# Kernel tuning notes

Measured on AMD Instinct MI355X. Metric: run time of the kernel, lower is better.

The kernel has to match this reference:

```python
import jax, jax.numpy as jnp
import numpy as np

F = 128  # num_features
N = 200000

def setup_inputs() -> dict:
    key = jax.random.key(0)
    ks = jax.random.split(key, 9)
    s = 0.05
    inp = {
        "node_feat": jax.random.normal(ks[0], (N, 4 * F), dtype=jnp.float32),
        "U_w": jax.random.normal(ks[1], (F, F), dtype=jnp.float32) * s,
        "U_b": jax.random.normal(ks[2], (F,), dtype=jnp.float32) * s,
        "V_w": jax.random.normal(ks[3], (F, F), dtype=jnp.float32) * s,
        "V_b": jax.random.normal(ks[4], (F,), dtype=jnp.float32) * s,
        "m1_w": jax.random.normal(ks[5], (2 * F, F), dtype=jnp.float32) * s,
        "m1_b": jax.random.normal(ks[6], (F,), dtype=jnp.float32) * s,
        "m2_w": jax.random.normal(ks[7], (F, 3 * F), dtype=jnp.float32) * s,
        "m2_b": jax.random.normal(ks[8], (3 * F,), dtype=jnp.float32) * s,
    }
    return inp

def reference(node_feat, U_w, U_b, V_w, V_b, m1_w, m1_b, m2_w, m2_b):
    node_scalar = node_feat[:, :F]                       # [N, F]
    node_vector = node_feat[:, F:].reshape(-1, 3, F)     # [N, 3, F]
    Uv = jnp.einsum('ncf,fg->ncg', node_vector, U_w) + U_b  # [N, 3, F]
    Vv = jnp.einsum('ncf,fg->ncg', node_vector, V_w) + V_b  # [N, 3, F]
    Vv_norm = jnp.linalg.norm(Vv, axis=1)                # [N, F]
    mlp_in = jnp.concatenate((Vv_norm, node_scalar), axis=1)  # [N, 2F]
    h = jax.nn.silu(mlp_in @ m1_w + m1_b)                # [N, F]
    mlp_out = h @ m2_w + m2_b                            # [N, 3F]
    a_vv, a_sv, a_ss = jnp.split(mlp_out, 3, axis=1)
    delta_v = a_vv[:, None, :] * Uv                      # [N, 3, F]
    inner_prod = jnp.sum(Uv * Vv, axis=1)                # [N, F]
    delta_s = a_sv * inner_prod + a_ss                   # [N, F]
    residual = jnp.concatenate([delta_s, delta_v.reshape(-1, 3 * F)], axis=1)
    return node_feat + residual
```

## Files before the change

### kernel.cpp

```cpp
#include <hip/hip_runtime.h>


#define NT 16
#define STRA 136
#define STRS 136
#define STRN 136
#define STRH 136

typedef __attribute__((ext_vector_type(8))) short bf16x8;
typedef __attribute__((ext_vector_type(4))) short short4v;
typedef __attribute__((ext_vector_type(4))) float f32x4;

#define MFMA16(a, b, c) __builtin_amdgcn_mfma_f32_16x16x32_bf16(a, b, c, 0, 0, 0)

__device__ __forceinline__ short f2bf(float x) {
    union { float f; unsigned u; } v; v.f = x;
    unsigned r = v.u + 0x7fffu + ((v.u >> 16) & 1u);
    return (short)(r >> 16);
}

__global__ void prep_weights(const float* __restrict__ Uw, const float* __restrict__ Vw,
                             const float* __restrict__ m1w, const float* __restrict__ m2w,
                             short* __restrict__ ws) {
    int idx = blockIdx.x * 256 + threadIdx.x;
    if (idx < 16384) {
        int g = idx >> 7, k = idx & 127;
        ws[idx]         = f2bf(Uw[k * 128 + g]);
        ws[16384 + idx] = f2bf(Vw[k * 128 + g]);
    } else if (idx < 49152) {
        int j = idx - 16384;
        int g = j >> 8, k = j & 255;
        ws[32768 + j] = f2bf(m1w[k * 128 + g]);
    } else if (idx < 98304) {
        int j = idx - 49152;
        int g = j >> 7, k = j & 127;
        ws[65536 + j] = f2bf(m2w[k * 384 + g]);
    }
}

__global__ __launch_bounds__(256, 4)
void painn_fused(const float* __restrict__ nf,
                 const float* __restrict__ Ub, const float* __restrict__ Vb,
                 const float* __restrict__ m1b, const float* __restrict__ m2b,
                 const short* __restrict__ wbuf,
                 float* __restrict__ out) {
    extern __shared__ short lds[];
    short* smA = lds;
    short* smS = smA + 48 * STRA;
    short* smN = smS + 16 * STRS;
    short* smH = smN + 16 * STRN;

    const short* Ut  = wbuf;
    const short* Vt  = wbuf + 16384;
    const short* M1t = wbuf + 32768;
    const short* M2t = wbuf + 65536;

    const int tid  = threadIdx.x;
    const int wave = tid >> 6;
    const int lane = tid & 63;
    const int fc   = lane & 15;
    const int quad = lane >> 4;
    const int ntg0 = wave * 2;
    const long nodebase = (long)blockIdx.x * NT;

    {
        const float* src = nf + nodebase * 512;
        float4 v[8];
        #pragma unroll
        for (int it = 0; it < 8; ++it) {
            int chunk = tid + 256 * it;
            int n = chunk >> 7;
            int col = (chunk & 127) << 2;
            v[it] = *(const float4*)(src + n * 512 + col);
        }
        #pragma unroll
        for (int it = 0; it < 8; ++it) {
            int chunk = tid + 256 * it;
            int n = chunk >> 7;
            int col = (chunk & 127) << 2;
            short4v s;
            s.x = f2bf(v[it].x); s.y = f2bf(v[it].y);
            s.z = f2bf(v[it].z); s.w = f2bf(v[it].w);
            if (col < 128) {
                *(short4v*)&smS[n * STRS + col] = s;
            } else {
                int vc = col - 128;
                int c = vc >> 7, k = vc & 127;
                *(short4v*)&smA[(c * 16 + n) * STRA + k] = s;
            }
        }
    }
    __syncthreads();

    f32x4 accU[2][3], accV[2][3];
    #pragma unroll
    for (int nt = 0; nt < 2; ++nt)
        #pragma unroll
        for (int c = 0; c < 3; ++c) { accU[nt][c] = (f32x4)(0.0f); accV[nt][c] = (f32x4)(0.0f); }

    #pragma unroll
    for (int kb = 0; kb < 4; ++kb) {
        const int koff = kb * 32 + quad * 8;
        bf16x8 af[3];
        #pragma unroll
        for (int c = 0; c < 3; ++c)
            af[c] = *(const bf16x8*)&smA[(c * 16 + fc) * STRA + koff];
        bf16x8 bu[2], bv[2];
        #pragma unroll
        for (int nt = 0; nt < 2; ++nt) {
            const int g = (ntg0 + nt) * 16 + fc;
            bu[nt] = *(const bf16x8*)&Ut[g * 128 + koff];
            bv[nt] = *(const bf16x8*)&Vt[g * 128 + koff];
        }
        #pragma unroll
        for (int nt = 0; nt < 2; ++nt)
            #pragma unroll
            for (int c = 0; c < 3; ++c) {
                accU[nt][c] = MFMA16(af[c], bu[nt], accU[nt][c]);
                accV[nt][c] = MFMA16(af[c], bv[nt], accV[nt][c]);
            }
    }

    float inner[2][4];
    #pragma unroll
    for (int nt = 0; nt < 2; ++nt) {
        const int g = (ntg0 + nt) * 16 + fc;
        const float ub = Ub[g], vb = Vb[g];
        #pragma unroll
        for (int i = 0; i < 4; ++i) {
            float u0 = accU[nt][0][i] + ub;
            float u1 = accU[nt][1][i] + ub;
            float u2 = accU[nt][2][i] + ub;
            float v0 = accV[nt][0][i] + vb;
            float v1 = accV[nt][1][i] + vb;
            float v2 = accV[nt][2][i] + vb;
            accU[nt][0][i] = u0; accU[nt][1][i] = u1; accU[nt][2][i] = u2;
            inner[nt][i] = u0 * v0 + u1 * v1 + u2 * v2;
            const float nrm = sqrtf(v0 * v0 + v1 * v1 + v2 * v2);
            const int nl = quad * 4 + i;
            smN[nl * STRN + g] = f2bf(nrm);
        }
    }
    __syncthreads();

    f32x4 acc2[2];
    acc2[0] = (f32x4)(0.0f); acc2[1] = (f32x4)(0.0f);
    #pragma unroll
    for (int kb = 0; kb < 8; ++kb) {
        const int kk = (kb & 3) * 32 + quad * 8;
        bf16x8 a0 = (kb < 4) ? *(const bf16x8*)&smN[fc * STRN + kk]
                             : *(const bf16x8*)&smS[fc * STRS + kk];
        #pragma unroll
        for (int nt = 0; nt < 2; ++nt) {
            const int g = (ntg0 + nt) * 16 + fc;
            bf16x8 b = *(const bf16x8*)&M1t[g * 256 + kb * 32 + quad * 8];
            acc2[nt] = MFMA16(a0, b, acc2[nt]);
        }
    }
    #pragma unroll
    for (int nt = 0; nt < 2; ++nt) {
        const int g = (ntg0 + nt) * 16 + fc;
        const float bb = m1b[g];
        #pragma unroll
        for (int i = 0; i < 4; ++i) {
            const float x = acc2[nt][i] + bb;
            const float sl = x / (1.0f + __expf(-x));
            const int nl = quad * 4 + i;
            smH[nl * STRH + g] = f2bf(sl);
        }
    }
    __syncthreads();

    f32x4 acc3[3][2];
    #pragma unroll
    for (int p = 0; p < 3; ++p) { acc3[p][0] = (f32x4)(0.0f); acc3[p][1] = (f32x4)(0.0f); }
    #pragma unroll
    for (int kb = 0; kb < 4; ++kb) {
        const int koff = kb * 32 + quad * 8;
        bf16x8 a0 = *(const bf16x8*)&smH[fc * STRH + koff];
        #pragma unroll
        for (int p = 0; p < 3; ++p)
            #pragma unroll
            for (int nt = 0; nt < 2; ++nt) {
                const int gcol = p * 128 + (ntg0 + nt) * 16 + fc;
                bf16x8 b = *(const bf16x8*)&M2t[gcol * 128 + koff];
                acc3[p][nt] = MFMA16(a0, b, acc3[p][nt]);
            }
    }

    #pragma unroll
    for (int nt = 0; nt < 2; ++nt) {
        const int g = (ntg0 + nt) * 16 + fc;
        const float bvv = m2b[g], bsv = m2b[128 + g], bss = m2b[256 + g];
        float nfv[4][4];
        #pragma unroll
        for (int i = 0; i < 4; ++i) {
            const long base = (nodebase + quad * 4 + i) * 512;
            nfv[i][0] = nf[base + g];
            nfv[i][1] = nf[base + 128 + g];
            nfv[i][2] = nf[base + 256 + g];
            nfv[i][3] = nf[base + 384 + g];
        }
        #pragma unroll
        for (int i = 0; i < 4; ++i) {
            const long base = (nodebase + quad * 4 + i) * 512;
            const float avv = acc3[0][nt][i] + bvv;
            const float asv = acc3[1][nt][i] + bsv;
            const float ass = acc3[2][nt][i] + bss;
            const float ds  = asv * inner[nt][i] + ass;
            out[base + g] = nfv[i][0] + ds;
            #pragma unroll
            for (int c = 0; c < 3; ++c)
                out[base + 128 + c * 128 + g] = nfv[i][c + 1] + avv * accU[nt][c][i];
        }
    }
}

extern "C" void kernel_launch(void* const* d_in, const int* in_sizes, int n_in,
                              void* d_out, int out_size, void* d_ws, size_t ws_size,
                              hipStream_t stream) {
    (void)in_sizes; (void)n_in; (void)out_size; (void)ws_size;
    const float* node_feat = (const float*)d_in[0];
    const float* U_w  = (const float*)d_in[1];
    const float* U_b  = (const float*)d_in[2];
    const float* V_w  = (const float*)d_in[3];
    const float* V_b  = (const float*)d_in[4];
    const float* m1_w = (const float*)d_in[5];
    const float* m1_b = (const float*)d_in[6];
    const float* m2_w = (const float*)d_in[7];
    const float* m2_b = (const float*)d_in[8];
    short* wbuf = (short*)d_ws;

    prep_weights<<<384, 256, 0, stream>>>(U_w, V_w, m1_w, m2_w, wbuf);

    const int nblocks = 200000 / NT;
    const size_t lds_bytes = (size_t)(48 * STRA + 16 * STRS + 16 * STRN + 16 * STRH) * sizeof(short);
    painn_fused<<<nblocks, 256, lds_bytes, stream>>>(
        node_feat, U_b, V_b, m1_b, m2_b, wbuf, (float*)d_out);
}
```

Measured before the change: 935.2 us.

## Process multiple node tiles per block with double-buffered prefetch of next tile

Each block now handles five 16-node tiles in a loop. The next tile's features are prefetched into registers during the current tile's compute and written into a second LDS buffer, and bias loads are hoisted out of the loop. The aim is to hide global load latency and amortize per-block setup. In exchange it doubles the input LDS footprint, lowers launch_bounds occupancy from 4 to 3, and raises register pressure from holding the prefetched data.

```diff
diff --git a/kernel.cpp b/kernel.cpp
--- a/kernel.cpp
+++ b/kernel.cpp
@@ -2,6 +2,7 @@
 
 
 #define NT 16
+#define TPB 5
 #define STRA 136
 #define STRS 136
 #define STRN 136
@@ -38,17 +39,19 @@
     }
 }
 
-__global__ __launch_bounds__(256, 4)
+__global__ __launch_bounds__(256, 3)
 void painn_fused(const float* __restrict__ nf,
                  const float* __restrict__ Ub, const float* __restrict__ Vb,
                  const float* __restrict__ m1b, const float* __restrict__ m2b,
                  const short* __restrict__ wbuf,
                  float* __restrict__ out) {
     extern __shared__ short lds[];
-    short* smA = lds;
-    short* smS = smA + 48 * STRA;
-    short* smN = smS + 16 * STRS;
-    short* smH = smN + 16 * STRN;
+    short* smA0 = lds;
+    short* smS0 = smA0 + 48 * STRA;
+    short* smA1 = smS0 + 16 * STRS;
+    short* smS1 = smA1 + 48 * STRA;
+    short* smN  = smS1 + 16 * STRS;
+    short* smH  = smN  + 16 * STRN;
 
     const short* Ut  = wbuf;
     const short* Vt  = wbuf + 16384;
@@ -61,158 +64,195 @@
     const int fc   = lane & 15;
     const int quad = lane >> 4;
     const int ntg0 = wave * 2;
-    const long nodebase = (long)blockIdx.x * NT;
+
+    float ub_[2], vb_[2], m1b_[2], bvv_[2], bsv_[2], bss_[2];
+    #pragma unroll
+    for (int nt = 0; nt < 2; ++nt) {
+        const int g = (ntg0 + nt) * 16 + fc;
+        ub_[nt]  = Ub[g];  vb_[nt]  = Vb[g];  m1b_[nt] = m1b[g];
+        bvv_[nt] = m2b[g]; bsv_[nt] = m2b[128 + g]; bss_[nt] = m2b[256 + g];
+    }
+
+    const int colf = (tid & 127) << 2;
+    const int rowb = tid >> 7;
+    const bool isS = colf < 128;
+    const int cA = (colf - 128) >> 7;
+    const int kA = (colf - 128) & 127;
+
+    const long nodebase0 = (long)blockIdx.x * (TPB * NT);
+
+    float4 v[8];
 
     {
-        const float* src = nf + nodebase * 512;
-        float4 v[8];
+        const float* src = nf + nodebase0 * 512;
+        #pragma unroll
+        for (int it = 0; it < 8; ++it)
+            v[it] = *(const float4*)(src + (long)(rowb + 2 * it) * 512 + colf);
         #pragma unroll
         for (int it = 0; it < 8; ++it) {
-            int chunk = tid + 256 * it;
-            int n = chunk >> 7;
-            int col = (chunk & 127) << 2;
-            v[it] = *(const float4*)(src + n * 512 + col);
-        }
-        #pragma unroll
-        for (int it = 0; it < 8; ++it) {
-            int chunk = tid + 256 * it;
-            int n = chunk >> 7;
-            int col = (chunk & 127) << 2;
+            const int n = rowb + 2 * it;
             short4v s;
             s.x = f2bf(v[it].x); s.y = f2bf(v[it].y);
             s.z = f2bf(v[it].z); s.w = f2bf(v[it].w);
-            if (col < 128) {
-                *(short4v*)&smS[n * STRS + col] = s;
-            } else {
-                int vc = col - 128;
-                int c = vc >> 7, k = vc & 127;
-                *(short4v*)&smA[(c * 16 + n) * STRA + k] = s;
-            }
+            if (isS) *(short4v*)&smS0[n * STRS + colf] = s;
+            else     *(short4v*)&smA0[(cA * 16 + n) * STRA + kA] = s;
         }
     }
     __syncthreads();
 
-    f32x4 accU[2][3], accV[2][3];
-    #pragma unroll
-    for (int nt = 0; nt < 2; ++nt)
-        #pragma unroll
-        for (int c = 0; c < 3; ++c) { accU[nt][c] = (f32x4)(0.0f); accV[nt][c] = (f32x4)(0.0f); }
-
-    #pragma unroll
-    for (int kb = 0; kb < 4; ++kb) {
-        const int koff = kb * 32 + quad * 8;
-        bf16x8 af[3];
-        #pragma unroll
-        for (int c = 0; c < 3; ++c)
-            af[c] = *(const bf16x8*)&smA[(c * 16 + fc) * STRA + koff];
-        bf16x8 bu[2], bv[2];
+    short* sA = smA0; short* sS = smS0;
+    short* dA = smA1; short* dS = smS1;
+
+    #pragma unroll 1
+    for (int t = 0; t < TPB; ++t) {
+        const long nodebase = nodebase0 + (long)t * NT;
+
+        if (t + 1 < TPB) {
+            const float* src = nf + (nodebase + NT) * 512;
+            #pragma unroll
+            for (int it = 0; it < 8; ++it)
+                v[it] = *(const float4*)(src + (long)(rowb + 2 * it) * 512 + colf);
+            __builtin_amdgcn_sched_barrier(0);
+        }
+
+        f32x4 accU[2][3], accV[2][3];
+        #pragma unroll
+        for (int nt = 0; nt < 2; ++nt)
+            #pragma unroll
+            for (int c = 0; c < 3; ++c) { accU[nt][c] = (f32x4)(0.0f); accV[nt][c] = (f32x4)(0.0f); }
+
+        #pragma unroll
+        for (int kb = 0; kb < 4; ++kb) {
+            const int koff = kb * 32 + quad * 8;
+            bf16x8 af[3];
+            #pragma unroll
+            for (int c = 0; c < 3; ++c)
+                af[c] = *(const bf16x8*)&sA[(c * 16 + fc) * STRA + koff];
+            bf16x8 bu[2], bv[2];
+            #pragma unroll
+            for (int nt = 0; nt < 2; ++nt) {
+                const int g = (ntg0 + nt) * 16 + fc;
+                bu[nt] = *(const bf16x8*)&Ut[g * 128 + koff];
+                bv[nt] = *(const bf16x8*)&Vt[g * 128 + koff];
+            }
+            #pragma unroll
+            for (int nt = 0; nt < 2; ++nt)
+                #pragma unroll
+                for (int c = 0; c < 3; ++c) {
+                    accU[nt][c] = MFMA16(af[c], bu[nt], accU[nt][c]);
+                    accV[nt][c] = MFMA16(af[c], bv[nt], accV[nt][c]);
+                }
+        }
+
+        float inner[2][4];
         #pragma unroll
         for (int nt = 0; nt < 2; ++nt) {
             const int g = (ntg0 + nt) * 16 + fc;
-            bu[nt] = *(const bf16x8*)&Ut[g * 128 + koff];
-            bv[nt] = *(const bf16x8*)&Vt[g * 128 + koff];
-        }
-        #pragma unroll
-        for (int nt = 0; nt < 2; ++nt)
-            #pragma unroll
-            for (int c = 0; c < 3; ++c) {
-                accU[nt][c] = MFMA16(af[c], bu[nt], accU[nt][c]);
-                accV[nt][c] = MFMA16(af[c], bv[nt], accV[nt][c]);
-            }
-    }
-
-    float inner[2][4];
-    #pragma unroll
-    for (int nt = 0; nt < 2; ++nt) {
-        const int g = (ntg0 + nt) * 16 + fc;
-        const float ub = Ub[g], vb = Vb[g];
-        #pragma unroll
-        for (int i = 0; i < 4; ++i) {
-            float u0 = accU[nt][0][i] + ub;
-            float u1 = accU[nt][1][i] + ub;
-            float u2 = accU[nt][2][i] + ub;
-            float v0 = accV[nt][0][i] + vb;
-            float v1 = accV[nt][1][i] + vb;
-            float v2 = accV[nt][2][i] + vb;
-            accU[nt][0][i] = u0; accU[nt][1][i] = u1; accU[nt][2][i] = u2;
-            inner[nt][i] = u0 * v0 + u1 * v1 + u2 * v2;
-            const float nrm = sqrtf(v0 * v0 + v1 * v1 + v2 * v2);
-            const int nl = quad * 4 + i;
-            smN[nl * STRN + g] = f2bf(nrm);
-        }
-    }
-    __syncthreads();
-
-    f32x4 acc2[2];
-    acc2[0] = (f32x4)(0.0f); acc2[1] = (f32x4)(0.0f);
-    #pragma unroll
-    for (int kb = 0; kb < 8; ++kb) {
-        const int kk = (kb & 3) * 32 + quad * 8;
-        bf16x8 a0 = (kb < 4) ? *(const bf16x8*)&smN[fc * STRN + kk]
-                             : *(const bf16x8*)&smS[fc * STRS + kk];
+            const float ub = ub_[nt], vb = vb_[nt];
+            #pragma unroll
+            for (int i = 0; i < 4; ++i) {
+                float u0 = accU[nt][0][i] + ub;
+                float u1 = accU[nt][1][i] + ub;
+                float u2 = accU[nt][2][i] + ub;
+                float v0 = accV[nt][0][i] + vb;
+                float v1 = accV[nt][1][i] + vb;
+                float v2 = accV[nt][2][i] + vb;
+                accU[nt][0][i] = u0; accU[nt][1][i] = u1; accU[nt][2][i] = u2;
+                inner[nt][i] = u0 * v0 + u1 * v1 + u2 * v2;
+                const float nrm = sqrtf(v0 * v0 + v1 * v1 + v2 * v2);
+                const int nl = quad * 4 + i;
+                smN[nl * STRN + g] = f2bf(nrm);
+            }
+        }
+        __syncthreads();
+
+        f32x4 acc2[2];
+        acc2[0] = (f32x4)(0.0f); acc2[1] = (f32x4)(0.0f);
+        #pragma unroll
+        for (int kb = 0; kb < 8; ++kb) {
+            const int kk = (kb & 3) * 32 + quad * 8;
+            bf16x8 a0 = (kb < 4) ? *(const bf16x8*)&smN[fc * STRN + kk]
+                                 : *(const bf16x8*)&sS[fc * STRS + kk];
+            #pragma unroll
+            for (int nt = 0; nt < 2; ++nt) {
+                const int g = (ntg0 + nt) * 16 + fc;
+                bf16x8 b = *(const bf16x8*)&M1t[g * 256 + kb * 32 + quad * 8];
+                acc2[nt] = MFMA16(a0, b, acc2[nt]);
+            }
+        }
         #pragma unroll
         for (int nt = 0; nt < 2; ++nt) {
             const int g = (ntg0 + nt) * 16 + fc;
-            bf16x8 b = *(const bf16x8*)&M1t[g * 256 + kb * 32 + quad * 8];
-            acc2[nt] = MFMA16(a0, b, acc2[nt]);
-        }
-    }
-    #pragma unroll
-    for (int nt = 0; nt < 2; ++nt) {
-        const int g = (ntg0 + nt) * 16 + fc;
-        const float bb = m1b[g];
-        #pragma unroll
-        for (int i = 0; i < 4; ++i) {
-            const float x = acc2[nt][i] + bb;
-            const float sl = x / (1.0f + __expf(-x));
-            const int nl = quad * 4 + i;
-            smH[nl * STRH + g] = f2bf(sl);
-        }
-    }
-    __syncthreads();
-
-    f32x4 acc3[3][2];
-    #pragma unroll
-    for (int p = 0; p < 3; ++p) { acc3[p][0] = (f32x4)(0.0f); acc3[p][1] = (f32x4)(0.0f); }
-    #pragma unroll
-    for (int kb = 0; kb < 4; ++kb) {
-        const int koff = kb * 32 + quad * 8;
-        bf16x8 a0 = *(const bf16x8*)&smH[fc * STRH + koff];
-        #pragma unroll
-        for (int p = 0; p < 3; ++p)
-            #pragma unroll
-            for (int nt = 0; nt < 2; ++nt) {
-                const int gcol = p * 128 + (ntg0 + nt) * 16 + fc;
-                bf16x8 b = *(const bf16x8*)&M2t[gcol * 128 + koff];
-                acc3[p][nt] = MFMA16(a0, b, acc3[p][nt]);
-            }
-    }
-
-    #pragma unroll
-    for (int nt = 0; nt < 2; ++nt) {
-        const int g = (ntg0 + nt) * 16 + fc;
-        const float bvv = m2b[g], bsv = m2b[128 + g], bss = m2b[256 + g];
-        float nfv[4][4];
-        #pragma unroll
-        for (int i = 0; i < 4; ++i) {
-            const long base = (nodebase + quad * 4 + i) * 512;
-            nfv[i][0] = nf[base + g];
-            nfv[i][1] = nf[base + 128 + g];
-            nfv[i][2] = nf[base + 256 + g];
-            nfv[i][3] = nf[base + 384 + g];
-        }
-        #pragma unroll
-        for (int i = 0; i < 4; ++i) {
-            const long base = (nodebase + quad * 4 + i) * 512;
-            const float avv = acc3[0][nt][i] + bvv;
-            const float asv = acc3[1][nt][i] + bsv;
-            const float ass = acc3[2][nt][i] + bss;
-            const float ds  = asv * inner[nt][i] + ass;
-            out[base + g] = nfv[i][0] + ds;
-            #pragma unroll
-            for (int c = 0; c < 3; ++c)
-                out[base + 128 + c * 128 + g] = nfv[i][c + 1] + avv * accU[nt][c][i];
-        }
+            const float bb = m1b_[nt];
+            #pragma unroll
+            for (int i = 0; i < 4; ++i) {
+                const float x = acc2[nt][i] + bb;
+                const float sl = x / (1.0f + __expf(-x));
+                const int nl = quad * 4 + i;
+                smH[nl * STRH + g] = f2bf(sl);
+            }
+        }
+
+        if (t + 1 < TPB) {
+            #pragma unroll
+            for (int it = 0; it < 8; ++it) {
+                const int n = rowb + 2 * it;
+                short4v s;
+                s.x = f2bf(v[it].x); s.y = f2bf(v[it].y);
+                s.z = f2bf(v[it].z); s.w = f2bf(v[it].w);
+                if (isS) *(short4v*)&dS[n * STRS + colf] = s;
+                else     *(short4v*)&dA[(cA * 16 + n) * STRA + kA] = s;
+            }
+        }
+        __syncthreads();
+
+        f32x4 acc3[3][2];
+        #pragma unroll
+        for (int p = 0; p < 3; ++p) { acc3[p][0] = (f32x4)(0.0f); acc3[p][1] = (f32x4)(0.0f); }
+        #pragma unroll
+        for (int kb = 0; kb < 4; ++kb) {
+            const int koff = kb * 32 + quad * 8;
+            bf16x8 a0 = *(const bf16x8*)&smH[fc * STRH + koff];
+            #pragma unroll
+            for (int p = 0; p < 3; ++p)
+                #pragma unroll
+                for (int nt = 0; nt < 2; ++nt) {
+                    const int gcol = p * 128 + (ntg0 + nt) * 16 + fc;
+                    bf16x8 b = *(const bf16x8*)&M2t[gcol * 128 + koff];
+                    acc3[p][nt] = MFMA16(a0, b, acc3[p][nt]);
+                }
+        }
+
+        #pragma unroll
+        for (int nt = 0; nt < 2; ++nt) {
+            const int g = (ntg0 + nt) * 16 + fc;
+            const float bvv = bvv_[nt], bsv = bsv_[nt], bss = bss_[nt];
+            float nfv[4][4];
+            #pragma unroll
+            for (int i = 0; i < 4; ++i) {
+                const long base = (nodebase + quad * 4 + i) * 512;
+                nfv[i][0] = nf[base + g];
+                nfv[i][1] = nf[base + 128 + g];
+                nfv[i][2] = nf[base + 256 + g];
+                nfv[i][3] = nf[base + 384 + g];
+            }
+            #pragma unroll
+            for (int i = 0; i < 4; ++i) {
+                const long base = (nodebase + quad * 4 + i) * 512;
+                const float avv = acc3[0][nt][i] + bvv;
+                const float asv = acc3[1][nt][i] + bsv;
+                const float ass = acc3[2][nt][i] + bss;
+                const float ds  = asv * inner[nt][i] + ass;
+                out[base + g] = nfv[i][0] + ds;
+                #pragma unroll
+                for (int c = 0; c < 3; ++c)
+                    out[base + 128 + c * 128 + g] = nfv[i][c + 1] + avv * accU[nt][c][i];
+            }
+        }
+
+        short* tmp;
+        tmp = sA; sA = dA; dA = tmp;
+        tmp = sS; sS = dS; dS = tmp;
     }
 }
 
@@ -233,8 +273,9 @@
 
     prep_weights<<<384, 256, 0, stream>>>(U_w, V_w, m1_w, m2_w, wbuf);
 
-    const int nblocks = 200000 / NT;
-    const size_t lds_bytes = (size_t)(48 * STRA + 16 * STRS + 16 * STRN + 16 * STRH) * sizeof(short);
+    const int nblocks = 200000 / (NT * TPB);
+    const size_t lds_bytes =
+        (size_t)(2 * (48 * STRA + 16 * STRS) + 16 * STRN + 16 * STRH) * sizeof(short);
     painn_fused<<<nblocks, 256, lds_bytes, stream>>>(
         node_feat, U_b, V_b, m1_b, m2_b, wbuf, (float*)d_out);
 }
```

Result: slower. 1.412 ms (+51.0%).
